# Optimization experiments

Measured on AMD Instinct MI355X. Metric: run time of the kernel, lower is better.

Reference implementation:

```python
import jax, jax.numpy as jnp
import numpy as np

EPS = 1e-6  # cell eps
LN_EPS = 1e-5  # torch LayerNorm default


def layer_norm(x, gamma, beta):
    mu = jnp.mean(x, axis=-1, keepdims=True)
    var = jnp.mean(jnp.square(x - mu), axis=-1, keepdims=True)
    return (x - mu) * jax.lax.rsqrt(var + LN_EPS) * gamma + beta


def normalized_exp_gate(pre):
    centered = pre - jnp.mean(pre, axis=1, keepdims=True)
    e = jnp.exp(jnp.clip(centered, -5.0, 5.0))
    return e / (jnp.sum(e, axis=1, keepdims=True) + EPS)


def setup_inputs() -> dict:
    key = jax.random.key(0)
    B, Din, H = 8192, 512, 1024
    ks = jax.random.split(key, 16)
    std = 1.0 / np.sqrt(H)
    u = lambda k, shape: jax.random.uniform(k, shape, jnp.float32, -std, std)
    return {
        "x": jax.random.normal(ks[0], (B, Din), jnp.float32),
        "h_prev": jax.random.normal(ks[1], (B, H), jnp.float32),
        "c_prev": jax.random.normal(ks[2], (B, H), jnp.float32),
        "Wx": u(ks[3], (4 * H, Din)),
        "bx": u(ks[4], (4 * H,)),
        "Wh": u(ks[5], (4 * H, H)),
        "bh": u(ks[6], (4 * H,)),
        "ln_in_g": u(ks[7], (4 * H,)),
        "ln_in_b": u(ks[8], (4 * H,)),
        "ln_hu_g": u(ks[9], (4 * H,)),
        "ln_hu_b": u(ks[10], (4 * H,)),
        "ln_c_g": u(ks[11], (H,)),
        "ln_c_b": u(ks[12], (H,)),
        "ln_h_g": u(ks[13], (H,)),
        "ln_h_b": u(ks[14], (H,)),
    }


def reference(x, h_prev, c_prev, Wx, bx, Wh, bh,
              ln_in_g, ln_in_b, ln_hu_g, ln_hu_b,
              ln_c_g, ln_c_b, ln_h_g, ln_h_b):
    # dropout p=0 -> identity (eval mode)
    gates_x = layer_norm(x @ Wx.T + bx, ln_in_g, ln_in_b)      # [B, 4H]
    gates_h = layer_norm(h_prev @ Wh.T + bh, ln_hu_g, ln_hu_b)  # [B, 4H]
    gates = gates_x + gates_h
    i, f, g, o = jnp.split(gates, 4, axis=1)
    i = normalized_exp_gate(i)
    f = normalized_exp_gate(f)
    gate_sum = i + f
    i = i / (gate_sum + EPS)
    f = f / (gate_sum + EPS)
    c_tilde = jnp.tanh(g)
    c = layer_norm(f * c_prev + i * c_tilde, ln_c_g, ln_c_b)
    o = jax.nn.sigmoid(o)
    c_out = layer_norm(jnp.tanh(c), ln_h_g, ln_h_b)
    h = o * c_out
    return (h, c)
```

## Files before the change

### kernel.cpp

```cpp
#include <hip/hip_runtime.h>
#include <hip/hip_bf16.h>
#include <stdint.h>
#include <math.h>

#define EPS_CELL 1e-6f
#define LN_EPS   1e-5f

typedef short short8 __attribute__((ext_vector_type(8)));
typedef float f32x4 __attribute__((ext_vector_type(4)));
typedef unsigned short ushort;

__device__ __forceinline__ ushort f2bf(float f) {
    union { float f; uint32_t u; } v; v.f = f;
    uint32_t r = v.u + 0x7FFFu + ((v.u >> 16) & 1u);
    return (ushort)(r >> 16);
}
__device__ __forceinline__ float bfbits2f(uint32_t hi16_in_place) {
    union { uint32_t u; float f; } v; v.u = hi16_in_place;
    return v.f;
}

__device__ __forceinline__ float fexp(float x)  { return __builtin_amdgcn_exp2f(x * 1.4426950408889634f); }
__device__ __forceinline__ float frcp(float x)  { return __builtin_amdgcn_rcpf(x); }
__device__ __forceinline__ float frsq(float x)  { return __builtin_amdgcn_rsqf(x); }
__device__ __forceinline__ float ftanh(float x) {
    float xc = fminf(fmaxf(x, -15.f), 15.f);
    float t  = fexp(2.f * xc);
    return (t - 1.f) * frcp(t + 1.f);
}
__device__ __forceinline__ float fsigm(float x) { return frcp(1.f + fexp(-x)); }

__global__ __launch_bounds__(256) void cast_all(
        const float* __restrict__ x,  const float* __restrict__ h,
        const float* __restrict__ wx, const float* __restrict__ wh,
        ushort* __restrict__ xb, ushort* __restrict__ hb,
        ushort* __restrict__ wxb, ushort* __restrict__ whb) {
    long i = ((long)blockIdx.x * 256 + threadIdx.x) * 8;
    const float* src; ushort* dst; long off;
    if      (i <  4194304L) { src = x;  dst = xb;  off = i; }
    else if (i < 12582912L) { src = h;  dst = hb;  off = i - 4194304L; }
    else if (i < 14680064L) { src = wx; dst = wxb; off = i - 12582912L; }
    else                    { src = wh; dst = whb; off = i - 14680064L; }
    const float4* p = (const float4*)(src + off);
    float4 a = p[0], b = p[1];
    uint4 r;
    r.x = (uint32_t)f2bf(a.x) | ((uint32_t)f2bf(a.y) << 16);
    r.y = (uint32_t)f2bf(a.z) | ((uint32_t)f2bf(a.w) << 16);
    r.z = (uint32_t)f2bf(b.x) | ((uint32_t)f2bf(b.y) << 16);
    r.w = (uint32_t)f2bf(b.z) | ((uint32_t)f2bf(b.w) << 16);
    *(uint4*)(dst + off) = r;
}

#define BAR()        __builtin_amdgcn_s_barrier()
#define SPRIO(x)     __builtin_amdgcn_s_setprio(x)
#define WAIT_LGKM0() do { asm volatile("s_waitcnt lgkmcnt(0)" ::: "memory"); \
                          __builtin_amdgcn_sched_barrier(0); } while (0)
#define WAIT_VM6()   do { asm volatile("s_waitcnt vmcnt(6)" ::: "memory"); \
                          __builtin_amdgcn_sched_barrier(0); } while (0)
#define WAIT_VM0()   do { asm volatile("s_waitcnt vmcnt(0)" ::: "memory"); \
                          __builtin_amdgcn_sched_barrier(0); } while (0)

template<int K>
__global__ __launch_bounds__(512, 2) void gemm256_8ph(
        const ushort* __restrict__ Ag,
        const ushort* __restrict__ Bg,
        const float*  __restrict__ bias,
        ushort* __restrict__ C,
        int GN, int m_base) {
    constexpr int NT = K / 64;
    constexpr int NP = NT / 2;

    __shared__ ushort lds[65536];

    const int t    = threadIdx.x;
    const int lane = t & 63;
    const int w    = t >> 6;
    const int wr   = w >> 2;
    const int wc   = w & 3;
    const int ln   = lane & 15;
    const int hi   = lane >> 4;
    const int sx   = ln & 7;

    const int bid = blockIdx.x;
    const int cpx = gridDim.x >> 3;
    const int wg  = (bid & 7) * cpx + (bid >> 3);
    const int n0  = (wg & 15) * 256;
    const int m0  = (wg >> 4) * 256 + m_base;

    const int trow = t >> 3;
    const int scol = (((t & 7) ^ (trow & 7)) * 8);

#define STG_A(buf, j, kb) __builtin_amdgcn_global_load_lds( \
    (const __attribute__((address_space(1))) void*)(Ag + (size_t)(m0 + (j)*64 + trow) * K + (kb) + scol), \
    (__attribute__((address_space(3))) void*)(lds + (buf)*32768 + (j)*4096 + t*8), 16, 0, 0)
#define STG_B(buf, j, kb) __builtin_amdgcn_global_load_lds( \
    (const __attribute__((address_space(1))) void*)(Bg + (size_t)(n0 + (j)*64 + trow) * K + (kb) + scol), \
    (__attribute__((address_space(3))) void*)(lds + (buf)*32768 + 16384 + (j)*4096 + t*8), 16, 0, 0)

    const int ca0  = ((0 + hi) ^ sx) * 8;
    const int ca1  = ((4 + hi) ^ sx) * 8;
    const int arow = (wr * 16 + ln) * 64;
    const int brow = (wc * 16 + ln) * 64 + 16384;

    short8 af[2][4], bf0[2][2], bf1[2][2];
    f32x4  acc[8][4] = {};

#define LD_A(buf, mbase) do { _Pragma("unroll") for (int m = 0; m < 4; ++m) { \
    af[0][m] = *(const short8*)&lds[(buf)*32768 + arow + ((mbase)+m)*2048 + ca0]; \
    af[1][m] = *(const short8*)&lds[(buf)*32768 + arow + ((mbase)+m)*2048 + ca1]; } } while (0)
#define LD_B(dst, buf, nbase) do { _Pragma("unroll") for (int n = 0; n < 2; ++n) { \
    dst[0][n] = *(const short8*)&lds[(buf)*32768 + brow + ((nbase)+n)*4096 + ca0]; \
    dst[1][n] = *(const short8*)&lds[(buf)*32768 + brow + ((nbase)+n)*4096 + ca1]; } } while (0)
#define MMQ(mb, nb, B_) do { _Pragma("unroll") for (int kk = 0; kk < 2; ++kk) \
    _Pragma("unroll") for (int m = 0; m < 4; ++m) \
    _Pragma("unroll") for (int n = 0; n < 2; ++n) \
        acc[(mb)+m][(nb)+n] = __builtin_amdgcn_mfma_f32_16x16x32_bf16( \
            af[kk][m], B_[kk][n], acc[(mb)+m][(nb)+n], 0, 0, 0); } while (0)

    STG_B(0,0,0);  STG_B(0,1,0);
    STG_A(0,0,0);  STG_A(0,1,0);
    STG_B(0,2,0);  STG_B(0,3,0);
    STG_A(0,2,0);  STG_A(0,3,0);
    STG_B(1,0,64); STG_B(1,1,64);
    STG_A(1,0,64); STG_A(1,1,64);
    STG_B(1,2,64); STG_B(1,3,64);
    WAIT_VM6(); BAR();

    for (int p = 0; p < NP; ++p) {
        const int k1 = (2*p + 1) * 64;
        const int t2 = (2*p + 2 < NT) ? (2*p + 2) : (2*p);
        const int t3 = (2*p + 3 < NT) ? (2*p + 3) : (2*p + 1);
        const int k2 = t2 * 64, k3 = t3 * 64;

        LD_A(0, 0); LD_B(bf0, 0, 0);
        STG_A(1,2,k1); STG_A(1,3,k1);
        BAR(); WAIT_LGKM0();
        SPRIO(1); MMQ(0,0,bf0); SPRIO(0); BAR();
        LD_B(bf1, 0, 2);
        STG_B(0,0,k2); STG_B(0,1,k2);
        BAR(); WAIT_LGKM0();
        SPRIO(1); MMQ(0,2,bf1); SPRIO(0); BAR();
        LD_A(0, 4);
        STG_A(0,0,k2); STG_A(0,1,k2);
        BAR(); WAIT_LGKM0();
        SPRIO(1); MMQ(4,0,bf0); SPRIO(0); BAR();
        STG_B(0,2,k2); STG_B(0,3,k2);
        BAR();
        SPRIO(1); MMQ(4,2,bf1); SPRIO(0);
        WAIT_VM6(); BAR();
        LD_A(1, 0); LD_B(bf0, 1, 0);
        STG_A(0,2,k2); STG_A(0,3,k2);
        BAR(); WAIT_LGKM0();
        SPRIO(1); MMQ(0,0,bf0); SPRIO(0); BAR();
        LD_B(bf1, 1, 2);
        STG_B(1,0,k3); STG_B(1,1,k3);
        BAR(); WAIT_LGKM0();
        SPRIO(1); MMQ(0,2,bf1); SPRIO(0); BAR();
        LD_A(1, 4);
        STG_A(1,0,k3); STG_A(1,1,k3);
        BAR(); WAIT_LGKM0();
        SPRIO(1); MMQ(4,0,bf0); SPRIO(0); BAR();
        STG_B(1,2,k3); STG_B(1,3,k3);
        BAR();
        SPRIO(1); MMQ(4,2,bf1); SPRIO(0);
        WAIT_VM6(); BAR();
    }

    WAIT_VM0();
    BAR();
#pragma unroll
    for (int n = 0; n < 4; ++n) {
        int cl   = n * 64 + wc * 16 + ln;
        float bv = bias[n0 + cl];
#pragma unroll
        for (int m = 0; m < 8; ++m) {
#pragma unroll
            for (int r = 0; r < 4; ++r) {
                int row = m * 32 + wr * 16 + hi * 4 + r;
                int sc  = (cl & 7) + ((((cl >> 3) ^ (row & 7))) << 3);
                lds[row * 256 + sc] = f2bf(acc[m][n][r] + bv);
            }
        }
    }
    BAR();
    {
        const int rr = t >> 5;
        const int oc = (t & 31) * 8;
#pragma unroll
        for (int i = 0; i < 16; ++i) {
            int row = i * 16 + rr;
            int sc  = (((oc >> 3) ^ (row & 7)) << 3);
            uint4 vv = *(const uint4*)&lds[row * 256 + sc];
            *(uint4*)(C + (size_t)(m0 + row) * GN + n0 + oc) = vv;
        }
    }
#undef STG_A
#undef STG_B
#undef LD_A
#undef LD_B
#undef MMQ
}

template<int NV>
__device__ __forceinline__ void row_reduce(float* v, float* slice) {
    const int lane = threadIdx.x & 63;
    const int wir  = (threadIdx.x >> 6) & 3;
#pragma unroll
    for (int i = 0; i < NV; ++i) {
        float s = v[i];
#pragma unroll
        for (int m = 32; m > 0; m >>= 1) s += __shfl_xor(s, m, 64);
        if (lane == 0) slice[i * 4 + wir] = s;
    }
    __syncthreads();
#pragma unroll
    for (int i = 0; i < NV; ++i)
        v[i] = slice[i * 4 + 0] + slice[i * 4 + 1] + slice[i * 4 + 2] + slice[i * 4 + 3];
}

__global__ __launch_bounds__(1024) void fused_cell4(
        const ushort* __restrict__ U, const ushort* __restrict__ V,
        const float* __restrict__ c_prev,
        const float* __restrict__ g_in, const float* __restrict__ b_in,
        const float* __restrict__ g_hu, const float* __restrict__ b_hu,
        const float* __restrict__ g_c,  const float* __restrict__ b_c,
        const float* __restrict__ g_h,  const float* __restrict__ b_h,
        float* __restrict__ out_h, float* __restrict__ out_c) {
    __shared__ float sred[4][4][16];
    const int t  = threadIdx.x;
    const int rr = t >> 8;
    const int tt = t & 255;
    const int r  = blockIdx.x * 4 + rr;
    const size_t rowG = (size_t)r * 4096;
    const size_t rowH = (size_t)r * 1024;
    const int c0 = tt * 4;

    uint2 uu[4], vv[4];
#pragma unroll
    for (int q = 0; q < 4; ++q) {
        uu[q] = *(const uint2*)(U + rowG + q * 1024 + c0);
        vv[q] = *(const uint2*)(V + rowG + q * 1024 + c0);
    }
    float4 cp4 = *(const float4*)(c_prev + rowH + c0);
    float4 gc4 = *(const float4*)(g_c + c0);
    float4 bc4 = *(const float4*)(b_c + c0);
    float4 gh4 = *(const float4*)(g_h + c0);
    float4 bh4 = *(const float4*)(b_h + c0);

    float uq[4][4], vq[4][4];
#pragma unroll
    for (int q = 0; q < 4; ++q) {
        uq[q][0] = bfbits2f(uu[q].x << 16); uq[q][1] = bfbits2f(uu[q].x & 0xFFFF0000u);
        uq[q][2] = bfbits2f(uu[q].y << 16); uq[q][3] = bfbits2f(uu[q].y & 0xFFFF0000u);
        vq[q][0] = bfbits2f(vv[q].x << 16); vq[q][1] = bfbits2f(vv[q].x & 0xFFFF0000u);
        vq[q][2] = bfbits2f(vv[q].y << 16); vq[q][3] = bfbits2f(vv[q].y & 0xFFFF0000u);
    }

    float red[4] = {0.f, 0.f, 0.f, 0.f};
#pragma unroll
    for (int q = 0; q < 4; ++q)
#pragma unroll
        for (int j = 0; j < 4; ++j) {
            red[0] += uq[q][j]; red[1] += uq[q][j] * uq[q][j];
            red[2] += vq[q][j]; red[3] += vq[q][j] * vq[q][j];
        }
    row_reduce<4>(red, sred[rr][0]);
    const float inv4096 = 1.f / 4096.f;
    float mu_u = red[0] * inv4096, mu_v = red[2] * inv4096;
    float rs_u = frsq(red[1] * inv4096 - mu_u * mu_u + LN_EPS);
    float rs_v = frsq(red[3] * inv4096 - mu_v * mu_v + LN_EPS);

    float gate[4][4];
#pragma unroll
    for (int q = 0; q < 4; ++q) {
        int idx = q * 1024 + c0;
        float4 gi_ = *(const float4*)(g_in + idx);
        float4 bi_ = *(const float4*)(b_in + idx);
        float4 gh_ = *(const float4*)(g_hu + idx);
        float4 bh_ = *(const float4*)(b_hu + idx);
        float gia[4] = {gi_.x, gi_.y, gi_.z, gi_.w};
        float bia[4] = {bi_.x, bi_.y, bi_.z, bi_.w};
        float gha[4] = {gh_.x, gh_.y, gh_.z, gh_.w};
        float bha[4] = {bh_.x, bh_.y, bh_.z, bh_.w};
#pragma unroll
        for (int j = 0; j < 4; ++j) {
            float zu = (uq[q][j] - mu_u) * rs_u;
            float zv = (vq[q][j] - mu_v) * rs_v;
            gate[q][j] = zu * gia[j] + bia[j] + zv * gha[j] + bha[j];
        }
    }

    float ei[4], ef[4];
    red[0] = 0.f; red[1] = 0.f;
#pragma unroll
    for (int q = 0; q < 4; ++q) {
        ei[q] = fexp(fminf(fmaxf(gate[0][q], -20.f), 20.f));
        ef[q] = fexp(fminf(fmaxf(gate[1][q], -20.f), 20.f));
        red[0] += ei[q]; red[1] += ef[q];
    }
    row_reduce<2>(red, sred[rr][1]);
    float inv_si = frcp(red[0] + EPS_CELL);
    float inv_sf = frcp(red[1] + EPS_CELL);

    float cprev[4] = {cp4.x, cp4.y, cp4.z, cp4.w};
    float cpv[4];
    red[0] = 0.f; red[1] = 0.f;
#pragma unroll
    for (int q = 0; q < 4; ++q) {
        float in_ = ei[q] * inv_si;
        float fn_ = ef[q] * inv_sf;
        float den = frcp(in_ + fn_ + EPS_CELL);
        cpv[q] = fn_ * den * cprev[q] + in_ * den * ftanh(gate[2][q]);
        red[0] += cpv[q]; red[1] += cpv[q] * cpv[q];
    }
    row_reduce<2>(red, sred[rr][2]);
    const float inv1024 = 1.f / 1024.f;
    float mu_c = red[0] * inv1024;
    float rs_c = frsq(red[1] * inv1024 - mu_c * mu_c + LN_EPS);

    float cv[4], th[4];
    {
        float gca[4] = {gc4.x, gc4.y, gc4.z, gc4.w};
        float bca[4] = {bc4.x, bc4.y, bc4.z, bc4.w};
        red[0] = 0.f; red[1] = 0.f;
#pragma unroll
        for (int q = 0; q < 4; ++q) {
            cv[q] = (cpv[q] - mu_c) * rs_c * gca[q] + bca[q];
            th[q] = ftanh(cv[q]);
            red[0] += th[q]; red[1] += th[q] * th[q];
        }
    }
    {
        float4 o; o.x = cv[0]; o.y = cv[1]; o.z = cv[2]; o.w = cv[3];
        *(float4*)(out_c + rowH + c0) = o;
    }
    row_reduce<2>(red, sred[rr][3]);
    float mu_t = red[0] * inv1024;
    float rs_t = frsq(red[1] * inv1024 - mu_t * mu_t + LN_EPS);

    {
        float gha[4] = {gh4.x, gh4.y, gh4.z, gh4.w};
        float bha[4] = {bh4.x, bh4.y, bh4.z, bh4.w};
        float hv[4];
#pragma unroll
        for (int q = 0; q < 4; ++q) {
            float co = (th[q] - mu_t) * rs_t * gha[q] + bha[q];
            hv[q] = fsigm(gate[3][q]) * co;
        }
        float4 o; o.x = hv[0]; o.y = hv[1]; o.z = hv[2]; o.w = hv[3];
        *(float4*)(out_h + rowH + c0) = o;
    }
}

extern "C" void kernel_launch(void* const* d_in, const int* in_sizes, int n_in,
                              void* d_out, int out_size, void* d_ws, size_t ws_size,
                              hipStream_t stream) {
    const float* x       = (const float*)d_in[0];
    const float* h_prev  = (const float*)d_in[1];
    const float* c_prev  = (const float*)d_in[2];
    const float* Wx      = (const float*)d_in[3];
    const float* bx      = (const float*)d_in[4];
    const float* Wh      = (const float*)d_in[5];
    const float* bh      = (const float*)d_in[6];
    const float* ln_in_g = (const float*)d_in[7];
    const float* ln_in_b = (const float*)d_in[8];
    const float* ln_hu_g = (const float*)d_in[9];
    const float* ln_hu_b = (const float*)d_in[10];
    const float* ln_c_g  = (const float*)d_in[11];
    const float* ln_c_b  = (const float*)d_in[12];
    const float* ln_h_g  = (const float*)d_in[13];
    const float* ln_h_b  = (const float*)d_in[14];

    const int B = 8192, Din = 512, H = 1024, G = 4096;

    ushort* xb  = (ushort*)d_ws;
    ushort* hb  = xb  + (size_t)B * Din;
    ushort* wxb = hb  + (size_t)B * H;
    ushort* whb = wxb + (size_t)G * Din;
    ushort* U   = whb + (size_t)G * H;
    ushort* V   = U   + (size_t)B * G;

    cast_all<<<9216, 256, 0, stream>>>(x, h_prev, Wx, Wh, xb, hb, wxb, whb);

    gemm256_8ph<512> <<<dim3(512), 512, 0, stream>>>(xb, wxb, bx, U, G, 0);
    gemm256_8ph<1024><<<dim3(256), 512, 0, stream>>>(hb, whb, bh, V, G, 0);
    gemm256_8ph<1024><<<dim3(256), 512, 0, stream>>>(hb, whb, bh, V, G, 4096);

    float* out_h = (float*)d_out;
    float* out_c = out_h + (size_t)B * H;
    fused_cell4<<<B / 4, 1024, 0, stream>>>(U, V, c_prev,
                                            ln_in_g, ln_in_b, ln_hu_g, ln_hu_b,
                                            ln_c_g, ln_c_b, ln_h_g, ln_h_b,
                                            out_h, out_c);
}
```

Baseline: 239.1 us.

## Process two rows per 256-thread block in fused cell and split x-GEMM launch

The fused epilogue kernel moves from four rows per 1024-thread block to two rows per 256-thread block. Each thread handles both rows, so the LayerNorm gamma/beta vectors are loaded once and reused, and the paired reductions share one barrier each. This reduces the barrier scope and the repeated parameter loads, at the cost of more registers per thread. The x-projection GEMM is also split into two 256-block launches using a row offset, matching the h-projection GEMM's launch pattern.

New measurement: 213.9 us, median of 2. 1.12x faster.

```diff
diff --git a/kernel.cpp b/kernel.cpp
--- a/kernel.cpp
+++ b/kernel.cpp
@@ -202,23 +202,28 @@
 }
 
 template<int NV>
-__device__ __forceinline__ void row_reduce(float* v, float* slice) {
+__device__ __forceinline__ void reduce2(float* v0, float* v1, float* s0, float* s1) {
     const int lane = threadIdx.x & 63;
-    const int wir  = (threadIdx.x >> 6) & 3;
+    const int w    = threadIdx.x >> 6;
 #pragma unroll
     for (int i = 0; i < NV; ++i) {
-        float s = v[i];
-#pragma unroll
-        for (int m = 32; m > 0; m >>= 1) s += __shfl_xor(s, m, 64);
-        if (lane == 0) slice[i * 4 + wir] = s;
+        float a = v0[i], b = v1[i];
+#pragma unroll
+        for (int m = 32; m > 0; m >>= 1) {
+            a += __shfl_xor(a, m, 64);
+            b += __shfl_xor(b, m, 64);
+        }
+        if (lane == 0) { s0[i * 4 + w] = a; s1[i * 4 + w] = b; }
     }
     __syncthreads();
 #pragma unroll
-    for (int i = 0; i < NV; ++i)
-        v[i] = slice[i * 4 + 0] + slice[i * 4 + 1] + slice[i * 4 + 2] + slice[i * 4 + 3];
-}
-
-__global__ __launch_bounds__(1024) void fused_cell4(
+    for (int i = 0; i < NV; ++i) {
+        v0[i] = s0[i * 4 + 0] + s0[i * 4 + 1] + s0[i * 4 + 2] + s0[i * 4 + 3];
+        v1[i] = s1[i * 4 + 0] + s1[i * 4 + 1] + s1[i * 4 + 2] + s1[i * 4 + 3];
+    }
+}
+
+__global__ __launch_bounds__(256) void fused_cell2(
         const ushort* __restrict__ U, const ushort* __restrict__ V,
         const float* __restrict__ c_prev,
         const float* __restrict__ g_in, const float* __restrict__ b_in,
@@ -226,129 +231,163 @@
         const float* __restrict__ g_c,  const float* __restrict__ b_c,
         const float* __restrict__ g_h,  const float* __restrict__ b_h,
         float* __restrict__ out_h, float* __restrict__ out_c) {
-    __shared__ float sred[4][4][16];
+    __shared__ float sred[2][4][16];
     const int t  = threadIdx.x;
-    const int rr = t >> 8;
-    const int tt = t & 255;
-    const int r  = blockIdx.x * 4 + rr;
-    const size_t rowG = (size_t)r * 4096;
-    const size_t rowH = (size_t)r * 1024;
-    const int c0 = tt * 4;
-
-    uint2 uu[4], vv[4];
-#pragma unroll
-    for (int q = 0; q < 4; ++q) {
-        uu[q] = *(const uint2*)(U + rowG + q * 1024 + c0);
-        vv[q] = *(const uint2*)(V + rowG + q * 1024 + c0);
-    }
-    float4 cp4 = *(const float4*)(c_prev + rowH + c0);
+    const int c0 = t * 4;
+    const int rb = blockIdx.x * 2;
+
+    uint2 uu[2][4], vv[2][4];
+    float4 cp4[2];
+#pragma unroll
+    for (int rj = 0; rj < 2; ++rj) {
+        const size_t rowG = (size_t)(rb + rj) * 4096;
+#pragma unroll
+        for (int q = 0; q < 4; ++q) {
+            uu[rj][q] = *(const uint2*)(U + rowG + q * 1024 + c0);
+            vv[rj][q] = *(const uint2*)(V + rowG + q * 1024 + c0);
+        }
+        cp4[rj] = *(const float4*)(c_prev + (size_t)(rb + rj) * 1024 + c0);
+    }
     float4 gc4 = *(const float4*)(g_c + c0);
     float4 bc4 = *(const float4*)(b_c + c0);
     float4 gh4 = *(const float4*)(g_h + c0);
     float4 bh4 = *(const float4*)(b_h + c0);
 
-    float uq[4][4], vq[4][4];
+    float red0[4] = {0.f, 0.f, 0.f, 0.f};
+    float red1[4] = {0.f, 0.f, 0.f, 0.f};
+#pragma unroll
+    for (int rj = 0; rj < 2; ++rj) {
+        float* rd = rj ? red1 : red0;
+#pragma unroll
+        for (int q = 0; q < 4; ++q) {
+            float u0 = bfbits2f(uu[rj][q].x << 16), u1 = bfbits2f(uu[rj][q].x & 0xFFFF0000u);
+            float u2 = bfbits2f(uu[rj][q].y << 16), u3 = bfbits2f(uu[rj][q].y & 0xFFFF0000u);
+            float v0 = bfbits2f(vv[rj][q].x << 16), v1 = bfbits2f(vv[rj][q].x & 0xFFFF0000u);
+            float v2 = bfbits2f(vv[rj][q].y << 16), v3 = bfbits2f(vv[rj][q].y & 0xFFFF0000u);
+            rd[0] += u0 + u1 + u2 + u3;
+            rd[1] += u0 * u0 + u1 * u1 + u2 * u2 + u3 * u3;
+            rd[2] += v0 + v1 + v2 + v3;
+            rd[3] += v0 * v0 + v1 * v1 + v2 * v2 + v3 * v3;
+        }
+    }
+    reduce2<4>(red0, red1, sred[0][0], sred[1][0]);
+    const float inv4096 = 1.f / 4096.f;
+    float mu_u[2], rs_u[2], mu_v[2], rs_v[2];
+    mu_u[0] = red0[0] * inv4096; mu_v[0] = red0[2] * inv4096;
+    rs_u[0] = frsq(red0[1] * inv4096 - mu_u[0] * mu_u[0] + LN_EPS);
+    rs_v[0] = frsq(red0[3] * inv4096 - mu_v[0] * mu_v[0] + LN_EPS);
+    mu_u[1] = red1[0] * inv4096; mu_v[1] = red1[2] * inv4096;
+    rs_u[1] = frsq(red1[1] * inv4096 - mu_u[1] * mu_u[1] + LN_EPS);
+    rs_v[1] = frsq(red1[3] * inv4096 - mu_v[1] * mu_v[1] + LN_EPS);
+
+    float gate[2][4][4];
 #pragma unroll
     for (int q = 0; q < 4; ++q) {
-        uq[q][0] = bfbits2f(uu[q].x << 16); uq[q][1] = bfbits2f(uu[q].x & 0xFFFF0000u);
-        uq[q][2] = bfbits2f(uu[q].y << 16); uq[q][3] = bfbits2f(uu[q].y & 0xFFFF0000u);
-        vq[q][0] = bfbits2f(vv[q].x << 16); vq[q][1] = bfbits2f(vv[q].x & 0xFFFF0000u);
-        vq[q][2] = bfbits2f(vv[q].y << 16); vq[q][3] = bfbits2f(vv[q].y & 0xFFFF0000u);
-    }
-
-    float red[4] = {0.f, 0.f, 0.f, 0.f};
-#pragma unroll
-    for (int q = 0; q < 4; ++q)
-#pragma unroll
-        for (int j = 0; j < 4; ++j) {
-            red[0] += uq[q][j]; red[1] += uq[q][j] * uq[q][j];
-            red[2] += vq[q][j]; red[3] += vq[q][j] * vq[q][j];
-        }
-    row_reduce<4>(red, sred[rr][0]);
-    const float inv4096 = 1.f / 4096.f;
-    float mu_u = red[0] * inv4096, mu_v = red[2] * inv4096;
-    float rs_u = frsq(red[1] * inv4096 - mu_u * mu_u + LN_EPS);
-    float rs_v = frsq(red[3] * inv4096 - mu_v * mu_v + LN_EPS);
-
-    float gate[4][4];
-#pragma unroll
-    for (int q = 0; q < 4; ++q) {
-        int idx = q * 1024 + c0;
-        float4 gi_ = *(const float4*)(g_in + idx);
-        float4 bi_ = *(const float4*)(b_in + idx);
-        float4 gh_ = *(const float4*)(g_hu + idx);
-        float4 bh_ = *(const float4*)(b_hu + idx);
-        float gia[4] = {gi_.x, gi_.y, gi_.z, gi_.w};
-        float bia[4] = {bi_.x, bi_.y, bi_.z, bi_.w};
-        float gha[4] = {gh_.x, gh_.y, gh_.z, gh_.w};
-        float bha[4] = {bh_.x, bh_.y, bh_.z, bh_.w};
-#pragma unroll
-        for (int j = 0; j < 4; ++j) {
-            float zu = (uq[q][j] - mu_u) * rs_u;
-            float zv = (vq[q][j] - mu_v) * rs_v;
-            gate[q][j] = zu * gia[j] + bia[j] + zv * gha[j] + bha[j];
-        }
-    }
-
-    float ei[4], ef[4];
-    red[0] = 0.f; red[1] = 0.f;
-#pragma unroll
-    for (int q = 0; q < 4; ++q) {
-        ei[q] = fexp(fminf(fmaxf(gate[0][q], -20.f), 20.f));
-        ef[q] = fexp(fminf(fmaxf(gate[1][q], -20.f), 20.f));
-        red[0] += ei[q]; red[1] += ef[q];
-    }
-    row_reduce<2>(red, sred[rr][1]);
-    float inv_si = frcp(red[0] + EPS_CELL);
-    float inv_sf = frcp(red[1] + EPS_CELL);
-
-    float cprev[4] = {cp4.x, cp4.y, cp4.z, cp4.w};
-    float cpv[4];
-    red[0] = 0.f; red[1] = 0.f;
-#pragma unroll
-    for (int q = 0; q < 4; ++q) {
-        float in_ = ei[q] * inv_si;
-        float fn_ = ef[q] * inv_sf;
-        float den = frcp(in_ + fn_ + EPS_CELL);
-        cpv[q] = fn_ * den * cprev[q] + in_ * den * ftanh(gate[2][q]);
-        red[0] += cpv[q]; red[1] += cpv[q] * cpv[q];
-    }
-    row_reduce<2>(red, sred[rr][2]);
+        const int idx = q * 1024 + c0;
+        float4 ga = *(const float4*)(g_in + idx);
+        float4 ba = *(const float4*)(b_in + idx);
+        float4 gb = *(const float4*)(g_hu + idx);
+        float4 bb = *(const float4*)(b_hu + idx);
+        float gaa[4] = {ga.x, ga.y, ga.z, ga.w};
+        float baa[4] = {ba.x, ba.y, ba.z, ba.w};
+        float gba[4] = {gb.x, gb.y, gb.z, gb.w};
+        float bba[4] = {bb.x, bb.y, bb.z, bb.w};
+#pragma unroll
+        for (int rj = 0; rj < 2; ++rj) {
+            float uf[4], vf[4];
+            uf[0] = bfbits2f(uu[rj][q].x << 16); uf[1] = bfbits2f(uu[rj][q].x & 0xFFFF0000u);
+            uf[2] = bfbits2f(uu[rj][q].y << 16); uf[3] = bfbits2f(uu[rj][q].y & 0xFFFF0000u);
+            vf[0] = bfbits2f(vv[rj][q].x << 16); vf[1] = bfbits2f(vv[rj][q].x & 0xFFFF0000u);
+            vf[2] = bfbits2f(vv[rj][q].y << 16); vf[3] = bfbits2f(vv[rj][q].y & 0xFFFF0000u);
+#pragma unroll
+            for (int j = 0; j < 4; ++j) {
+                float zu = (uf[j] - mu_u[rj]) * rs_u[rj];
+                float zv = (vf[j] - mu_v[rj]) * rs_v[rj];
+                gate[rj][q][j] = zu * gaa[j] + baa[j] + zv * gba[j] + bba[j];
+            }
+        }
+    }
+
+    float ei[2][4], ef[2][4];
+    red0[0] = red0[1] = red1[0] = red1[1] = 0.f;
+#pragma unroll
+    for (int rj = 0; rj < 2; ++rj) {
+        float* rd = rj ? red1 : red0;
+#pragma unroll
+        for (int q = 0; q < 4; ++q) {
+            ei[rj][q] = fexp(fminf(fmaxf(gate[rj][0][q], -20.f), 20.f));
+            ef[rj][q] = fexp(fminf(fmaxf(gate[rj][1][q], -20.f), 20.f));
+            rd[0] += ei[rj][q]; rd[1] += ef[rj][q];
+        }
+    }
+    reduce2<2>(red0, red1, sred[0][1], sred[1][1]);
+    float inv_si[2], inv_sf[2];
+    inv_si[0] = frcp(red0[0] + EPS_CELL); inv_sf[0] = frcp(red0[1] + EPS_CELL);
+    inv_si[1] = frcp(red1[0] + EPS_CELL); inv_sf[1] = frcp(red1[1] + EPS_CELL);
+
+    float cpv[2][4];
+    red0[0] = red0[1] = red1[0] = red1[1] = 0.f;
+#pragma unroll
+    for (int rj = 0; rj < 2; ++rj) {
+        float* rd = rj ? red1 : red0;
+        float cpr[4] = {cp4[rj].x, cp4[rj].y, cp4[rj].z, cp4[rj].w};
+#pragma unroll
+        for (int q = 0; q < 4; ++q) {
+            float in_ = ei[rj][q] * inv_si[rj];
+            float fn_ = ef[rj][q] * inv_sf[rj];
+            float den = frcp(in_ + fn_ + EPS_CELL);
+            cpv[rj][q] = fn_ * den * cpr[q] + in_ * den * ftanh(gate[rj][2][q]);
+            rd[0] += cpv[rj][q]; rd[1] += cpv[rj][q] * cpv[rj][q];
+        }
+    }
+    reduce2<2>(red0, red1, sred[0][2], sred[1][2]);
     const float inv1024 = 1.f / 1024.f;
-    float mu_c = red[0] * inv1024;
-    float rs_c = frsq(red[1] * inv1024 - mu_c * mu_c + LN_EPS);
-
-    float cv[4], th[4];
+    float mu_c[2], rs_c[2];
+    mu_c[0] = red0[0] * inv1024;
+    rs_c[0] = frsq(red0[1] * inv1024 - mu_c[0] * mu_c[0] + LN_EPS);
+    mu_c[1] = red1[0] * inv1024;
+    rs_c[1] = frsq(red1[1] * inv1024 - mu_c[1] * mu_c[1] + LN_EPS);
+
+    float th[2][4];
     {
         float gca[4] = {gc4.x, gc4.y, gc4.z, gc4.w};
         float bca[4] = {bc4.x, bc4.y, bc4.z, bc4.w};
-        red[0] = 0.f; red[1] = 0.f;
-#pragma unroll
-        for (int q = 0; q < 4; ++q) {
-            cv[q] = (cpv[q] - mu_c) * rs_c * gca[q] + bca[q];
-            th[q] = ftanh(cv[q]);
-            red[0] += th[q]; red[1] += th[q] * th[q];
-        }
-    }
-    {
-        float4 o; o.x = cv[0]; o.y = cv[1]; o.z = cv[2]; o.w = cv[3];
-        *(float4*)(out_c + rowH + c0) = o;
-    }
-    row_reduce<2>(red, sred[rr][3]);
-    float mu_t = red[0] * inv1024;
-    float rs_t = frsq(red[1] * inv1024 - mu_t * mu_t + LN_EPS);
+        red0[0] = red0[1] = red1[0] = red1[1] = 0.f;
+#pragma unroll
+        for (int rj = 0; rj < 2; ++rj) {
+            float* rd = rj ? red1 : red0;
+            float cv[4];
+#pragma unroll
+            for (int q = 0; q < 4; ++q) {
+                cv[q] = (cpv[rj][q] - mu_c[rj]) * rs_c[rj] * gca[q] + bca[q];
+                th[rj][q] = ftanh(cv[q]);
+                rd[0] += th[rj][q]; rd[1] += th[rj][q] * th[rj][q];
+            }
+            float4 o; o.x = cv[0]; o.y = cv[1]; o.z = cv[2]; o.w = cv[3];
+            *(float4*)(out_c + (size_t)(rb + rj) * 1024 + c0) = o;
+        }
+    }
+    reduce2<2>(red0, red1, sred[0][3], sred[1][3]);
+    float mu_t[2], rs_t[2];
+    mu_t[0] = red0[0] * inv1024;
+    rs_t[0] = frsq(red0[1] * inv1024 - mu_t[0] * mu_t[0] + LN_EPS);
+    mu_t[1] = red1[0] * inv1024;
+    rs_t[1] = frsq(red1[1] * inv1024 - mu_t[1] * mu_t[1] + LN_EPS);
 
     {
         float gha[4] = {gh4.x, gh4.y, gh4.z, gh4.w};
         float bha[4] = {bh4.x, bh4.y, bh4.z, bh4.w};
-        float hv[4];
-#pragma unroll
-        for (int q = 0; q < 4; ++q) {
-            float co = (th[q] - mu_t) * rs_t * gha[q] + bha[q];
-            hv[q] = fsigm(gate[3][q]) * co;
-        }
-        float4 o; o.x = hv[0]; o.y = hv[1]; o.z = hv[2]; o.w = hv[3];
-        *(float4*)(out_h + rowH + c0) = o;
+#pragma unroll
+        for (int rj = 0; rj < 2; ++rj) {
+            float hv[4];
+#pragma unroll
+            for (int q = 0; q < 4; ++q) {
+                float co = (th[rj][q] - mu_t[rj]) * rs_t[rj] * gha[q] + bha[q];
+                hv[q] = fsigm(gate[rj][3][q]) * co;
+            }
+            float4 o; o.x = hv[0]; o.y = hv[1]; o.z = hv[2]; o.w = hv[3];
+            *(float4*)(out_h + (size_t)(rb + rj) * 1024 + c0) = o;
+        }
     }
 }
 
@@ -382,14 +421,15 @@
 
     cast_all<<<9216, 256, 0, stream>>>(x, h_prev, Wx, Wh, xb, hb, wxb, whb);
 
-    gemm256_8ph<512> <<<dim3(512), 512, 0, stream>>>(xb, wxb, bx, U, G, 0);
+    gemm256_8ph<512> <<<dim3(256), 512, 0, stream>>>(xb, wxb, bx, U, G, 0);
+    gemm256_8ph<512> <<<dim3(256), 512, 0, stream>>>(xb, wxb, bx, U, G, 4096);
     gemm256_8ph<1024><<<dim3(256), 512, 0, stream>>>(hb, whb, bh, V, G, 0);
     gemm256_8ph<1024><<<dim3(256), 512, 0, stream>>>(hb, whb, bh, V, G, 4096);
 
     float* out_h = (float*)d_out;
     float* out_c = out_h + (size_t)B * H;
-    fused_cell4<<<B / 4, 1024, 0, stream>>>(U, V, c_prev,
-                                            ln_in_g, ln_in_b, ln_hu_g, ln_hu_b,
-                                            ln_c_g, ln_c_b, ln_h_g, ln_h_b,
-                                            out_h, out_c);
-}
+    fused_cell2<<<B / 2, 256, 0, stream>>>(U, V, c_prev,
+                                           ln_in_g, ln_in_b, ln_hu_g, ln_hu_b,
+                                           ln_c_g, ln_c_b, ln_h_g, ln_h_b,
+                                           out_h, out_c);
+}
```
